# Performance work log

Measured on AMD Instinct MI355X. Metric: run time of the kernel, lower is better.

The kernel has to match this reference:

```python
import jax, jax.numpy as jnp
import numpy as np

N = 102400   # total nodes (64 graphs x 1600 nodes)
G = 64       # graphs in batch
NPG = N // G
E = 1638400  # total edges (avg degree 16)
EPG = E // G


def _segmean(x, ids, num):
    s = jax.ops.segment_sum(x, ids, num_segments=num)
    c = jax.ops.segment_sum(jnp.ones((x.shape[0], 1), x.dtype), ids, num_segments=num)
    return s / jnp.maximum(c, 1.0)


def setup_inputs() -> dict:
    key = jax.random.key(0)
    ks = jax.random.split(key, 32)
    node_features = jax.random.normal(ks[0], (N, 60), jnp.float32)
    edge_features = jax.random.normal(ks[1], (E, 1), jnp.float32)
    node_graph = jnp.arange(N, dtype=jnp.int32) // NPG
    edge_graph = jnp.arange(E, dtype=jnp.int32) // EPG
    senders = edge_graph * NPG + jax.random.randint(ks[2], (E,), 0, NPG)
    receivers = edge_graph * NPG + jax.random.randint(ks[3], (E,), 0, NPG)

    def W(k, o, i):
        return (jax.random.normal(k, (o, i), jnp.float32) / np.sqrt(i)).astype(jnp.float32)

    def b(k, o):
        return (jax.random.uniform(k, (o,), jnp.float32) * 0.02 - 0.01).astype(jnp.float32)

    p = dict(
        node_features=node_features, edge_features=edge_features,
        senders=senders, receivers=receivers,
        node_graph=node_graph, edge_graph=edge_graph,
        # encoder: EdgeLinear(8, edge=1, sender=60)
        enc_Wee=W(ks[4], 8, 1), enc_Wes=W(ks[5], 8, 60), enc_be=b(ks[6], 8),
        # encoder: NodeLinear(16, incoming=8, node=60)
        enc_Wnn=W(ks[7], 16, 60), enc_Wni=W(ks[8], 16, 8), enc_bn=b(ks[9], 16),
        # encoder: GlobalLinear(4, edge=8, node=16)
        enc_Wge=W(ks[10], 4, 8), enc_Wgn=W(ks[11], 4, 16), enc_bg=b(ks[12], 4),
        # hidden: EdgeLinear(8, edge=8, sender=16, global=4)
        hid_Wee=W(ks[13], 8, 8), hid_Wes=W(ks[14], 8, 16), hid_Weg=W(ks[15], 8, 4), hid_be=b(ks[16], 8),
        # hidden: NodeLinear(16, node=16, incoming=8, global=4)
        hid_Wnn=W(ks[17], 16, 16), hid_Wni=W(ks[18], 16, 8), hid_Wng=W(ks[19], 16, 4), hid_bn=b(ks[20], 16),
        # hidden: GlobalLinear(4, edge=8, node=16, global=4)
        hid_Wge=W(ks[21], 4, 8), hid_Wgn=W(ks[22], 4, 16), hid_Wgg=W(ks[23], 4, 4), hid_bg=b(ks[24], 4),
        # readouts
        ro_Wn=W(ks[25], 1, 16), ro_bn=b(ks[26], 1),
        ro_Wg=W(ks[27], 1, 4), ro_bg=b(ks[28], 1),
    )
    return p


def reference(node_features, edge_features, senders, receivers, node_graph, edge_graph,
              enc_Wee, enc_Wes, enc_be, enc_Wnn, enc_Wni, enc_bn, enc_Wge, enc_Wgn, enc_bg,
              hid_Wee, hid_Wes, hid_Weg, hid_be, hid_Wnn, hid_Wni, hid_Wng, hid_bn,
              hid_Wge, hid_Wgn, hid_Wgg, hid_bg, ro_Wn, ro_bn, ro_Wg, ro_bg):
    hops = 1
    # ---- encoder GN block ----
    e = jax.nn.relu(edge_features @ enc_Wee.T + node_features[senders] @ enc_Wes.T + enc_be)  # [E,8]
    n = jax.nn.relu(node_features @ enc_Wnn.T + _segmean(e, receivers, N) @ enc_Wni.T + enc_bn)  # [N,16]
    g = jax.nn.relu(_segmean(e, edge_graph, G) @ enc_Wge.T + _segmean(n, node_graph, G) @ enc_Wgn.T + enc_bg)  # [G,4]
    # ---- hidden GN blocks (shared weights across hops) ----
    for _ in range(hops):
        e = jax.nn.relu(e @ hid_Wee.T + n[senders] @ hid_Wes.T + g[edge_graph] @ hid_Weg.T + hid_be)
        n = jax.nn.relu(n @ hid_Wnn.T + _segmean(e, receivers, N) @ hid_Wni.T + g[node_graph] @ hid_Wng.T + hid_bn)
        g = jax.nn.relu(_segmean(e, edge_graph, G) @ hid_Wge.T + _segmean(n, node_graph, G) @ hid_Wgn.T + g @ hid_Wgg.T + hid_bg)
    # ---- readouts ----
    nodes_out = jax.nn.sigmoid(n @ ro_Wn.T + ro_bn)    # [N,1]
    globals_out = jax.nn.sigmoid(g @ ro_Wg.T + ro_bg)  # [G,1]
    return nodes_out, globals_out
```

## Files before the change

kernel.cpp:

```cpp
#include <hip/hip_runtime.h>
#include <hip/hip_bf16.h>
#include <hip/hip_fp16.h>

#define NN   102400
#define NG   64
#define NPG  1600
#define NE   1638400
#define EPG  25600
#define EPC  (EPG / 4)

typedef unsigned int u32;
typedef unsigned short u16;

#define OFF_EDAT  0
#define OFF_SPROJ (NE)
#define OFF_PNN   (NE + 8 * NN)
#define OFF_DEG   (NE + 16 * NN)
#define OFF_START (NE + 17 * NN)
#define OFF_H4C   (NE + 18 * NN)
#define OFF_GS    (NE + 22 * NN)
#define GS_ESUM1 0
#define GS_NSUM1 512
#define GS_ESUM2 1536
#define GS_NSUM2 2048
#define GS_G1    3072
#define GS_GPE   3328
#define GS_GPN   3840

struct H8 { __half2 a, b, c, d; };

__device__ __forceinline__ void unpack8(const H8 v, float* o) {
    float2 t0 = __half22float2(v.a), t1 = __half22float2(v.b);
    float2 t2 = __half22float2(v.c), t3 = __half22float2(v.d);
    o[0]=t0.x; o[1]=t0.y; o[2]=t1.x; o[3]=t1.y; o[4]=t2.x; o[5]=t2.y; o[6]=t3.x; o[7]=t3.y;
}
__device__ __forceinline__ H8 pack8(const float* v) {
    H8 r;
    r.a = __floats2half2_rn(v[0], v[1]); r.b = __floats2half2_rn(v[2], v[3]);
    r.c = __floats2half2_rn(v[4], v[5]); r.d = __floats2half2_rn(v[6], v[7]);
    return r;
}
__device__ __forceinline__ u16 f2bf(float f) {
    u32 u = __float_as_uint(f);
    return (u16)((u + 0x7fffu + ((u >> 16) & 1u)) >> 16);
}
__device__ __forceinline__ float wsum(float v) {
#pragma unroll
    for (int o = 32; o >= 1; o >>= 1) v += __shfl_xor(v, o);
    return v;
}
__device__ __forceinline__ float sigmoidf_(float x) { return 1.f / (1.f + expf(-x)); }

__global__ __launch_bounds__(512) void k_hist4(const int* __restrict__ rcv, int* __restrict__ h4) {
    __shared__ int h[NPG];
    const int g = blockIdx.x >> 2, c = blockIdx.x & 3;
    for (int i = threadIdx.x; i < NPG; i += 512) h[i] = 0;
    __syncthreads();
    const int base = g * EPG + c * EPC;
    for (int t = threadIdx.x; t < EPC; t += 512) atomicAdd(&h[rcv[base + t] - g * NPG], 1);
    __syncthreads();
    int* out = h4 + (size_t)(g * 4 + c) * NPG;
    for (int i = threadIdx.x; i < NPG; i += 512) out[i] = h[i];
}

__global__ __launch_bounds__(320) void k_scan(
    int* __restrict__ h4c, int* __restrict__ deg, int* __restrict__ start)
{
    __shared__ int part[320];
    const int g = blockIdx.x, tid = threadIdx.x;
    const int vb = tid * 5;
    int hc[5][4], d[5], pre[5];
    int ts = 0;
#pragma unroll
    for (int i = 0; i < 5; ++i) {
        const int v = vb + i;
#pragma unroll
        for (int c = 0; c < 4; ++c) hc[i][c] = h4c[(size_t)(g * 4 + c) * NPG + v];
        d[i] = hc[i][0] + hc[i][1] + hc[i][2] + hc[i][3];
        pre[i] = ts;
        ts += d[i];
    }
    part[tid] = ts;
    __syncthreads();
    for (int o = 1; o < 320; o <<= 1) {
        const int v = (tid >= o) ? part[tid - o] : 0;
        __syncthreads();
        part[tid] += v;
        __syncthreads();
    }
    const int off = g * EPG + part[tid] - ts;
#pragma unroll
    for (int i = 0; i < 5; ++i) {
        const int v = vb + i;
        const int st = off + pre[i];
        deg[g * NPG + v] = d[i];
        start[g * NPG + v] = st;
        int run = st;
#pragma unroll
        for (int c = 0; c < 4; ++c) {
            h4c[(size_t)(g * 4 + c) * NPG + v] = run;
            run += hc[i][c];
        }
    }
}

__global__ __launch_bounds__(512) void k_scatter4(
    const float* __restrict__ ef, const int* __restrict__ snd, const int* __restrict__ rcv,
    const int* __restrict__ h4c, u32* __restrict__ edat)
{
    __shared__ int cur[NPG];
    const int g = blockIdx.x >> 2, c = blockIdx.x & 3;
    const int* cb = h4c + (size_t)(g * 4 + c) * NPG;
    for (int i = threadIdx.x; i < NPG; i += 512) cur[i] = cb[i];
    __syncthreads();
    const int base = g * EPG + c * EPC;
    for (int t = threadIdx.x; t < EPC; t += 512) {
        const int e = base + t;
        const int r = rcv[e] - g * NPG;
        const int p = atomicAdd(&cur[r], 1);
        const u32 s = (u32)(snd[e] - g * NPG);
        edat[p] = (s << 16) | (u32)f2bf(ef[e]);
    }
}

__global__ __launch_bounds__(256) void k_node_pre(
    const float* __restrict__ nf,
    const float* __restrict__ Wes,
    const float* __restrict__ Wnn,
    const float* __restrict__ ebe, const float* __restrict__ ebn,
    __half* __restrict__ sproj, __half* __restrict__ pnn)
{
    __shared__ float wE[480], wN[960];
    for (int i = threadIdx.x; i < 480; i += 256) wE[i] = Wes[i];
    for (int i = threadIdx.x; i < 960; i += 256) wN[i] = Wnn[i];
    __syncthreads();
    const int v = blockIdx.x * 256 + threadIdx.x;
    const float4* row = reinterpret_cast<const float4*>(nf + (size_t)v * 60);
    float x[60];
#pragma unroll
    for (int i = 0; i < 15; ++i) {
        const float4 a = row[i];
        x[4 * i] = a.x; x[4 * i + 1] = a.y; x[4 * i + 2] = a.z; x[4 * i + 3] = a.w;
    }
    float pes[8], pn[16];
#pragma unroll
    for (int j = 0; j < 8; ++j) pes[j] = ebe[j];
#pragma unroll
    for (int j = 0; j < 16; ++j) pn[j] = ebn[j];
#pragma unroll
    for (int k = 0; k < 60; ++k) {
        const float xv = x[k];
#pragma unroll
        for (int j = 0; j < 8; ++j)  pes[j] = fmaf(xv, wE[j * 60 + k], pes[j]);
#pragma unroll
        for (int j = 0; j < 16; ++j) pn[j]  = fmaf(xv, wN[j * 60 + k], pn[j]);
    }
    H8* sp = reinterpret_cast<H8*>(sproj) + (size_t)v * 2;
    sp[0] = pack8(pes);
    H8* pp = reinterpret_cast<H8*>(pnn) + (size_t)v * 2;
    pp[0] = pack8(pn); pp[1] = pack8(pn + 8);
}

__global__ __launch_bounds__(256) void k_enc(
    const int* __restrict__ deg, const int* __restrict__ start, const u32* __restrict__ edat,
    __half* __restrict__ sproj, __half* __restrict__ pnn,
    const float* __restrict__ eWee,
    const float* __restrict__ eWni,
    const float* __restrict__ hWes, const float* __restrict__ hWnn,
    float* __restrict__ esum, float* __restrict__ nsum)
{
    __shared__ float wNI[128], wES[128], wNN2[256];
    for (int i = threadIdx.x; i < 128; i += 256) { wNI[i] = eWni[i]; wES[i] = hWes[i]; }
    for (int i = threadIdx.x; i < 256; i += 256) wNN2[i] = hWnn[i];
    __syncthreads();
    const int v = blockIdx.x * 256 + threadIdx.x;
    const int g = v / NPG;
    float wee[8];
#pragma unroll
    for (int j = 0; j < 8; ++j) wee[j] = eWee[j];
    const int dg = deg[v];
    const int st = start[v];
    float m[8];
#pragma unroll
    for (int j = 0; j < 8; ++j) m[j] = 0.f;
    const H8* hb = reinterpret_cast<const H8*>(sproj) + (size_t)g * NPG * 2;
    for (int i = 0; i < dg; ++i) {
        const u32 w = edat[st + i];
        const float f = __uint_as_float((w & 0xffffu) << 16);
        const int s = (int)(w >> 16);
        float pv[8]; unpack8(hb[(size_t)s * 2], pv);
#pragma unroll
        for (int j = 0; j < 8; ++j) m[j] += fmaxf(0.f, fmaf(f, wee[j], pv[j]));
    }
#pragma unroll
    for (int j = 0; j < 8; ++j) {
        const float t = wsum(m[j]);
        if ((threadIdx.x & 63) == 0) atomicAdd(&esum[g * 8 + j], t);
    }
    const float ic = 1.f / fmaxf((float)dg, 1.f);
    float mk[8];
#pragma unroll
    for (int k = 0; k < 8; ++k) mk[k] = m[k] * ic;
    const H8* pp = reinterpret_cast<const H8*>(pnn) + (size_t)v * 2;
    float pn[16]; unpack8(pp[0], pn); unpack8(pp[1], pn + 8);
    float n1[16];
#pragma unroll
    for (int j = 0; j < 16; ++j) {
        float x = pn[j];
#pragma unroll
        for (int k = 0; k < 8; ++k) x = fmaf(mk[k], wNI[j * 8 + k], x);
        n1[j] = fmaxf(0.f, x);
    }
    float pe[8];
#pragma unroll
    for (int o = 0; o < 8; ++o) {
        float x = 0.f;
#pragma unroll
        for (int j = 0; j < 16; ++j) x = fmaf(n1[j], wES[o * 16 + j], x);
        pe[o] = x;
    }
    H8* spw = reinterpret_cast<H8*>(sproj) + (size_t)v * 2;
    spw[1] = pack8(pe);
    float pw[16];
#pragma unroll
    for (int o = 0; o < 16; ++o) {
        float x = 0.f;
#pragma unroll
        for (int j = 0; j < 16; ++j) x = fmaf(n1[j], wNN2[o * 16 + j], x);
        pw[o] = x;
    }
    H8* ppw = reinterpret_cast<H8*>(pnn) + (size_t)v * 2;
    ppw[0] = pack8(pw); ppw[1] = pack8(pw + 8);
#pragma unroll
    for (int j = 0; j < 16; ++j) {
        const float t = wsum(n1[j]);
        if ((threadIdx.x & 63) == 0) atomicAdd(&nsum[g * 16 + j], t);
    }
}

__global__ void k_glob_enc(
    const float* __restrict__ esum1, const float* __restrict__ nsum1,
    const float* __restrict__ Wge, const float* __restrict__ Wgn, const float* __restrict__ bg,
    const float* __restrict__ hWeg, const float* __restrict__ hWng,
    float* __restrict__ g1, float* __restrict__ gpe, float* __restrict__ gpn)
{
    const int g = threadIdx.x;
    if (g >= NG) return;
    float gv[4];
#pragma unroll
    for (int o = 0; o < 4; ++o) {
        float x = bg[o];
#pragma unroll
        for (int k = 0; k < 8; ++k)  x = fmaf(esum1[g * 8 + k] * (1.f / EPG), Wge[o * 8 + k], x);
#pragma unroll
        for (int k = 0; k < 16; ++k) x = fmaf(nsum1[g * 16 + k] * (1.f / NPG), Wgn[o * 16 + k], x);
        gv[o] = fmaxf(0.f, x);
        g1[g * 4 + o] = gv[o];
    }
#pragma unroll
    for (int j = 0; j < 8; ++j) {
        float x = 0.f;
#pragma unroll
        for (int o = 0; o < 4; ++o) x = fmaf(gv[o], hWeg[j * 4 + o], x);
        gpe[g * 8 + j] = x;
    }
#pragma unroll
    for (int j = 0; j < 16; ++j) {
        float x = 0.f;
#pragma unroll
        for (int o = 0; o < 4; ++o) x = fmaf(gv[o], hWng[j * 4 + o], x);
        gpn[g * 16 + j] = x;
    }
}

__global__ __launch_bounds__(256) void k_hid(
    const int* __restrict__ deg, const int* __restrict__ start, const u32* __restrict__ edat,
    const __half* __restrict__ sproj, const __half* __restrict__ pnn,
    const float* __restrict__ eWee,
    const float* __restrict__ hWee, const float* __restrict__ hbe, const float* __restrict__ gpe,
    const float* __restrict__ hWni, const float* __restrict__ hbn, const float* __restrict__ gpn,
    const float* __restrict__ roWn, const float* __restrict__ robn,
    float* __restrict__ esum, float* __restrict__ nsum, float* __restrict__ outn)
{
    __shared__ float w2[64], wNI[128], rW[16];
    for (int i = threadIdx.x; i < 128; i += 256) wNI[i] = hWni[i];
    if (threadIdx.x < 64) w2[threadIdx.x] = hWee[threadIdx.x];
    if (threadIdx.x < 16) rW[threadIdx.x] = roWn[threadIdx.x];
    __syncthreads();
    const int v = blockIdx.x * 256 + threadIdx.x;
    const int g = v / NPG;
    float wee[8], add2[8];
#pragma unroll
    for (int j = 0; j < 8; ++j) { wee[j] = eWee[j]; add2[j] = gpe[g * 8 + j] + hbe[j]; }
    const int dg = deg[v];
    const int st = start[v];
    float m2[8];
#pragma unroll
    for (int j = 0; j < 8; ++j) m2[j] = 0.f;
    const H8* hb = reinterpret_cast<const H8*>(sproj) + (size_t)g * NPG * 2;
    for (int i = 0; i < dg; ++i) {
        const u32 w = edat[st + i];
        const float f = __uint_as_float((w & 0xffffu) << 16);
        const int s = (int)(w >> 16);
        float pv[8], qv[8];
        unpack8(hb[(size_t)s * 2], pv);
        unpack8(hb[(size_t)s * 2 + 1], qv);
        float e1[8];
#pragma unroll
        for (int j = 0; j < 8; ++j) e1[j] = fmaxf(0.f, fmaf(f, wee[j], pv[j]));
#pragma unroll
        for (int j = 0; j < 8; ++j) {
            float x = qv[j] + add2[j];
#pragma unroll
            for (int k = 0; k < 8; ++k) x = fmaf(e1[k], w2[j * 8 + k], x);
            m2[j] += fmaxf(0.f, x);
        }
    }
#pragma unroll
    for (int j = 0; j < 8; ++j) {
        const float t = wsum(m2[j]);
        if ((threadIdx.x & 63) == 0) atomicAdd(&esum[g * 8 + j], t);
    }
    const float ic = 1.f / fmaxf((float)dg, 1.f);
    float mk[8];
#pragma unroll
    for (int k = 0; k < 8; ++k) mk[k] = m2[k] * ic;
    const H8* pp = reinterpret_cast<const H8*>(pnn) + (size_t)v * 2;
    float pn[16]; unpack8(pp[0], pn); unpack8(pp[1], pn + 8);
    float z = robn[0];
    float n2[16];
#pragma unroll
    for (int j = 0; j < 16; ++j) {
        float x = pn[j] + gpn[g * 16 + j] + hbn[j];
#pragma unroll
        for (int k = 0; k < 8; ++k) x = fmaf(mk[k], wNI[j * 8 + k], x);
        n2[j] = fmaxf(0.f, x);
        z = fmaf(n2[j], rW[j], z);
    }
    outn[v] = sigmoidf_(z);
#pragma unroll
    for (int j = 0; j < 16; ++j) {
        const float t = wsum(n2[j]);
        if ((threadIdx.x & 63) == 0) atomicAdd(&nsum[g * 16 + j], t);
    }
}

__global__ void k_glob_hid(
    const float* __restrict__ esum2, const float* __restrict__ nsum2, const float* __restrict__ g1,
    const float* __restrict__ hWge, const float* __restrict__ hWgn,
    const float* __restrict__ hWgg, const float* __restrict__ hbg,
    const float* __restrict__ roWg, const float* __restrict__ robg,
    float* __restrict__ outg)
{
    const int g = threadIdx.x;
    if (g >= NG) return;
    float gv[4];
#pragma unroll
    for (int o = 0; o < 4; ++o) {
        float x = hbg[o];
#pragma unroll
        for (int k = 0; k < 8; ++k)  x = fmaf(esum2[g * 8 + k] * (1.f / EPG), hWge[o * 8 + k], x);
#pragma unroll
        for (int k = 0; k < 16; ++k) x = fmaf(nsum2[g * 16 + k] * (1.f / NPG), hWgn[o * 16 + k], x);
#pragma unroll
        for (int k = 0; k < 4; ++k)  x = fmaf(g1[g * 4 + k], hWgg[o * 4 + k], x);
        gv[o] = fmaxf(0.f, x);
    }
    float z = robg[0];
#pragma unroll
    for (int o = 0; o < 4; ++o) z = fmaf(gv[o], roWg[o], z);
    outg[g] = sigmoidf_(z);
}

extern "C" void kernel_launch(void* const* d_in, const int* in_sizes, int n_in,
                              void* d_out, int out_size, void* d_ws, size_t ws_size,
                              hipStream_t stream)
{
    const float* nf   = (const float*)d_in[0];
    const float* ef   = (const float*)d_in[1];
    const int*   snd  = (const int*)d_in[2];
    const int*   rcv  = (const int*)d_in[3];
    const float* eWee = (const float*)d_in[6];
    const float* eWes = (const float*)d_in[7];
    const float* ebe  = (const float*)d_in[8];
    const float* eWnn = (const float*)d_in[9];
    const float* eWni = (const float*)d_in[10];
    const float* ebn  = (const float*)d_in[11];
    const float* eWge = (const float*)d_in[12];
    const float* eWgn = (const float*)d_in[13];
    const float* ebg  = (const float*)d_in[14];
    const float* hWee = (const float*)d_in[15];
    const float* hWes = (const float*)d_in[16];
    const float* hWeg = (const float*)d_in[17];
    const float* hbe  = (const float*)d_in[18];
    const float* hWnn = (const float*)d_in[19];
    const float* hWni = (const float*)d_in[20];
    const float* hWng = (const float*)d_in[21];
    const float* hbn  = (const float*)d_in[22];
    const float* hWge = (const float*)d_in[23];
    const float* hWgn = (const float*)d_in[24];
    const float* hWgg = (const float*)d_in[25];
    const float* hbg  = (const float*)d_in[26];
    const float* roWn = (const float*)d_in[27];
    const float* robn = (const float*)d_in[28];
    const float* roWg = (const float*)d_in[29];
    const float* robg = (const float*)d_in[30];

    float*  ws    = (float*)d_ws;
    u32*    edat  = (u32*)(ws + OFF_EDAT);
    __half* sproj = (__half*)(ws + OFF_SPROJ);
    __half* pnn   = (__half*)(ws + OFF_PNN);
    int*    deg   = (int*)(ws + OFF_DEG);
    int*    start = (int*)(ws + OFF_START);
    int*    h4c   = (int*)(ws + OFF_H4C);
    float*  gs    = ws + OFF_GS;
    float* esum1 = gs + GS_ESUM1;
    float* nsum1 = gs + GS_NSUM1;
    float* esum2 = gs + GS_ESUM2;
    float* nsum2 = gs + GS_NSUM2;
    float* g1    = gs + GS_G1;
    float* gpe   = gs + GS_GPE;
    float* gpn   = gs + GS_GPN;
    float* out   = (float*)d_out;

    hipMemsetAsync(gs, 0, 3072 * sizeof(float), stream);

    k_hist4<<<NG * 4, 512, 0, stream>>>(rcv, h4c);
    k_scan<<<NG, 320, 0, stream>>>(h4c, deg, start);
    k_scatter4<<<NG * 4, 512, 0, stream>>>(ef, snd, rcv, h4c, edat);
    k_node_pre<<<NN / 256, 256, 0, stream>>>(nf, eWes, eWnn, ebe, ebn, sproj, pnn);
    k_enc<<<NN / 256, 256, 0, stream>>>(deg, start, edat, sproj, pnn,
                                        eWee, eWni, hWes, hWnn, esum1, nsum1);
    k_glob_enc<<<1, 64, 0, stream>>>(esum1, nsum1, eWge, eWgn, ebg, hWeg, hWng, g1, gpe, gpn);
    k_hid<<<NN / 256, 256, 0, stream>>>(deg, start, edat, sproj, pnn,
                                        eWee, hWee, hbe, gpe, hWni, hbn, gpn,
                                        roWn, robn, esum2, nsum2, out);
    k_glob_hid<<<1, 64, 0, stream>>>(esum2, nsum2, g1, hWge, hWgn, hWgg, hbg, roWg, robg, out + NN);
}
```

Baseline: 145.7 us.

## Split each node's edge gather across two threads and unroll gathers by four

The encoder and hidden node kernels now give each node to two threads. Each thread handles half the incoming edges, and the partial sums are combined with a lane shuffle; the per-node 16-wide projections are also split between the two threads. The edge loops are unrolled by four with the gathered loads issued up front, to raise memory-level parallelism on the random sender gathers. The global-sum memset is folded into the first block of k_node_pre, which removes one launch. The cost is twice as many threads, extra shuffles, and a modified wave reduction that relies on the lane pairing.

Measured after the change: 144.0 us. Within noise of the previous version (-1.1%).

```diff
diff --git a/kernel.cpp b/kernel.cpp
--- a/kernel.cpp
+++ b/kernel.cpp
@@ -28,6 +28,7 @@
 #define GS_GPN   3840
 
 struct H8 { __half2 a, b, c, d; };
+struct H4 { __half2 a, b; };
 
 __device__ __forceinline__ void unpack8(const H8 v, float* o) {
     float2 t0 = __half22float2(v.a), t1 = __half22float2(v.b);
@@ -40,13 +41,18 @@
     r.c = __floats2half2_rn(v[4], v[5]); r.d = __floats2half2_rn(v[6], v[7]);
     return r;
 }
+__device__ __forceinline__ H4 pack4(const float* v) {
+    H4 r;
+    r.a = __floats2half2_rn(v[0], v[1]); r.b = __floats2half2_rn(v[2], v[3]);
+    return r;
+}
 __device__ __forceinline__ u16 f2bf(float f) {
     u32 u = __float_as_uint(f);
     return (u16)((u + 0x7fffu + ((u >> 16) & 1u)) >> 16);
 }
-__device__ __forceinline__ float wsum(float v) {
-#pragma unroll
-    for (int o = 32; o >= 1; o >>= 1) v += __shfl_xor(v, o);
+__device__ __forceinline__ float wsum_par(float v) {
+#pragma unroll
+    for (int o = 2; o <= 32; o <<= 1) v += __shfl_xor(v, o);
     return v;
 }
 __device__ __forceinline__ float sigmoidf_(float x) { return 1.f / (1.f + expf(-x)); }
@@ -128,11 +134,14 @@
     const float* __restrict__ Wes,
     const float* __restrict__ Wnn,
     const float* __restrict__ ebe, const float* __restrict__ ebn,
-    __half* __restrict__ sproj, __half* __restrict__ pnn)
+    __half* __restrict__ sproj, __half* __restrict__ pnn, float* __restrict__ gs)
 {
     __shared__ float wE[480], wN[960];
     for (int i = threadIdx.x; i < 480; i += 256) wE[i] = Wes[i];
     for (int i = threadIdx.x; i < 960; i += 256) wN[i] = Wnn[i];
+    if (blockIdx.x == 0) {
+        for (int i = threadIdx.x; i < 3072; i += 256) gs[i] = 0.f;
+    }
     __syncthreads();
     const int v = blockIdx.x * 256 + threadIdx.x;
     const float4* row = reinterpret_cast<const float4*>(nf + (size_t)v * 60);
@@ -171,70 +180,99 @@
 {
     __shared__ float wNI[128], wES[128], wNN2[256];
     for (int i = threadIdx.x; i < 128; i += 256) { wNI[i] = eWni[i]; wES[i] = hWes[i]; }
-    for (int i = threadIdx.x; i < 256; i += 256) wNN2[i] = hWnn[i];
-    __syncthreads();
-    const int v = blockIdx.x * 256 + threadIdx.x;
+    wNN2[threadIdx.x] = hWnn[threadIdx.x];
+    __syncthreads();
+    const int t = blockIdx.x * 256 + threadIdx.x;
+    const int v = t >> 1, h = t & 1;
     const int g = v / NPG;
     float wee[8];
 #pragma unroll
     for (int j = 0; j < 8; ++j) wee[j] = eWee[j];
     const int dg = deg[v];
     const int st = start[v];
+    const int half0 = dg >> 1;
+    int i = st + (h ? half0 : 0);
+    const int iend = st + (h ? dg : half0);
     float m[8];
 #pragma unroll
     for (int j = 0; j < 8; ++j) m[j] = 0.f;
     const H8* hb = reinterpret_cast<const H8*>(sproj) + (size_t)g * NPG * 2;
-    for (int i = 0; i < dg; ++i) {
-        const u32 w = edat[st + i];
-        const float f = __uint_as_float((w & 0xffffu) << 16);
-        const int s = (int)(w >> 16);
-        float pv[8]; unpack8(hb[(size_t)s * 2], pv);
-#pragma unroll
-        for (int j = 0; j < 8; ++j) m[j] += fmaxf(0.f, fmaf(f, wee[j], pv[j]));
-    }
+
+#define ENC_EDGE(W, A) { \
+    const float f_ = __uint_as_float(((W) & 0xffffu) << 16); \
+    float pv_[8]; unpack8((A), pv_); \
+    _Pragma("unroll") \
+    for (int j = 0; j < 8; ++j) m[j] += fmaxf(0.f, fmaf(f_, wee[j], pv_[j])); }
+
+    for (; i + 4 <= iend; i += 4) {
+        const u32 w0 = edat[i], w1 = edat[i + 1], w2v = edat[i + 2], w3v = edat[i + 3];
+        const H8 A0 = hb[(size_t)(w0 >> 16) * 2];
+        const H8 A1 = hb[(size_t)(w1 >> 16) * 2];
+        const H8 A2 = hb[(size_t)(w2v >> 16) * 2];
+        const H8 A3 = hb[(size_t)(w3v >> 16) * 2];
+        ENC_EDGE(w0, A0) ENC_EDGE(w1, A1) ENC_EDGE(w2v, A2) ENC_EDGE(w3v, A3)
+    }
+    for (; i < iend; ++i) {
+        const u32 w = edat[i];
+        const H8 A = hb[(size_t)(w >> 16) * 2];
+        ENC_EDGE(w, A)
+    }
+#undef ENC_EDGE
+
+#pragma unroll
+    for (int j = 0; j < 8; ++j) m[j] += __shfl_xor(m[j], 1);
 #pragma unroll
     for (int j = 0; j < 8; ++j) {
-        const float t = wsum(m[j]);
-        if ((threadIdx.x & 63) == 0) atomicAdd(&esum[g * 8 + j], t);
+        const float s = wsum_par(m[j]);
+        if ((threadIdx.x & 63) == 0) atomicAdd(&esum[g * 8 + j], s);
     }
     const float ic = 1.f / fmaxf((float)dg, 1.f);
     float mk[8];
 #pragma unroll
     for (int k = 0; k < 8; ++k) mk[k] = m[k] * ic;
     const H8* pp = reinterpret_cast<const H8*>(pnn) + (size_t)v * 2;
-    float pn[16]; unpack8(pp[0], pn); unpack8(pp[1], pn + 8);
-    float n1[16];
-#pragma unroll
-    for (int j = 0; j < 16; ++j) {
-        float x = pn[j];
-#pragma unroll
-        for (int k = 0; k < 8; ++k) x = fmaf(mk[k], wNI[j * 8 + k], x);
-        n1[j] = fmaxf(0.f, x);
-    }
-    float pe[8];
-#pragma unroll
-    for (int o = 0; o < 8; ++o) {
+    float pn8[8]; unpack8(pp[h], pn8);
+    float n1[8];
+#pragma unroll
+    for (int jj = 0; jj < 8; ++jj) {
+        float x = pn8[jj];
+#pragma unroll
+        for (int k = 0; k < 8; ++k) x = fmaf(mk[k], wNI[(h * 8 + jj) * 8 + k], x);
+        n1[jj] = fmaxf(0.f, x);
+    }
+    float n1o[8];
+#pragma unroll
+    for (int jj = 0; jj < 8; ++jj) n1o[jj] = __shfl_xor(n1[jj], 1);
+    float full[16];
+#pragma unroll
+    for (int jj = 0; jj < 8; ++jj) {
+        full[jj]     = h ? n1o[jj] : n1[jj];
+        full[8 + jj] = h ? n1[jj]  : n1o[jj];
+    }
+    float pe4[4];
+#pragma unroll
+    for (int oo = 0; oo < 4; ++oo) {
+        const int o = h * 4 + oo;
         float x = 0.f;
 #pragma unroll
-        for (int j = 0; j < 16; ++j) x = fmaf(n1[j], wES[o * 16 + j], x);
-        pe[o] = x;
-    }
-    H8* spw = reinterpret_cast<H8*>(sproj) + (size_t)v * 2;
-    spw[1] = pack8(pe);
-    float pw[16];
-#pragma unroll
-    for (int o = 0; o < 16; ++o) {
+        for (int j = 0; j < 16; ++j) x = fmaf(full[j], wES[o * 16 + j], x);
+        pe4[oo] = x;
+    }
+    *reinterpret_cast<H4*>(sproj + (size_t)v * 16 + 8 + h * 4) = pack4(pe4);
+    float pw8[8];
+#pragma unroll
+    for (int oo = 0; oo < 8; ++oo) {
+        const int o = h * 8 + oo;
         float x = 0.f;
 #pragma unroll
-        for (int j = 0; j < 16; ++j) x = fmaf(n1[j], wNN2[o * 16 + j], x);
-        pw[o] = x;
-    }
-    H8* ppw = reinterpret_cast<H8*>(pnn) + (size_t)v * 2;
-    ppw[0] = pack8(pw); ppw[1] = pack8(pw + 8);
-#pragma unroll
-    for (int j = 0; j < 16; ++j) {
-        const float t = wsum(n1[j]);
-        if ((threadIdx.x & 63) == 0) atomicAdd(&nsum[g * 16 + j], t);
+        for (int j = 0; j < 16; ++j) x = fmaf(full[j], wNN2[o * 16 + j], x);
+        pw8[oo] = x;
+    }
+    reinterpret_cast<H8*>(pnn)[(size_t)v * 2 + h] = pack8(pw8);
+#pragma unroll
+    for (int jj = 0; jj < 8; ++jj) {
+        const float s = wsum_par(n1[jj]);
+        if ((threadIdx.x & 63) == h) atomicAdd(&nsum[g * 16 + h * 8 + jj], s);
     }
 }
 
@@ -287,61 +325,83 @@
     if (threadIdx.x < 64) w2[threadIdx.x] = hWee[threadIdx.x];
     if (threadIdx.x < 16) rW[threadIdx.x] = roWn[threadIdx.x];
     __syncthreads();
-    const int v = blockIdx.x * 256 + threadIdx.x;
+    const int t = blockIdx.x * 256 + threadIdx.x;
+    const int v = t >> 1, h = t & 1;
     const int g = v / NPG;
     float wee[8], add2[8];
 #pragma unroll
     for (int j = 0; j < 8; ++j) { wee[j] = eWee[j]; add2[j] = gpe[g * 8 + j] + hbe[j]; }
     const int dg = deg[v];
     const int st = start[v];
+    const int half0 = dg >> 1;
+    int i = st + (h ? half0 : 0);
+    const int iend = st + (h ? dg : half0);
     float m2[8];
 #pragma unroll
     for (int j = 0; j < 8; ++j) m2[j] = 0.f;
     const H8* hb = reinterpret_cast<const H8*>(sproj) + (size_t)g * NPG * 2;
-    for (int i = 0; i < dg; ++i) {
-        const u32 w = edat[st + i];
-        const float f = __uint_as_float((w & 0xffffu) << 16);
-        const int s = (int)(w >> 16);
-        float pv[8], qv[8];
-        unpack8(hb[(size_t)s * 2], pv);
-        unpack8(hb[(size_t)s * 2 + 1], qv);
-        float e1[8];
-#pragma unroll
-        for (int j = 0; j < 8; ++j) e1[j] = fmaxf(0.f, fmaf(f, wee[j], pv[j]));
-#pragma unroll
-        for (int j = 0; j < 8; ++j) {
-            float x = qv[j] + add2[j];
-#pragma unroll
-            for (int k = 0; k < 8; ++k) x = fmaf(e1[k], w2[j * 8 + k], x);
-            m2[j] += fmaxf(0.f, x);
-        }
-    }
+
+#define HID_EDGE(W, A, B) { \
+    const float f_ = __uint_as_float(((W) & 0xffffu) << 16); \
+    float pv_[8], qv_[8]; unpack8((A), pv_); unpack8((B), qv_); \
+    float e1_[8]; \
+    _Pragma("unroll") \
+    for (int j = 0; j < 8; ++j) e1_[j] = fmaxf(0.f, fmaf(f_, wee[j], pv_[j])); \
+    _Pragma("unroll") \
+    for (int j = 0; j < 8; ++j) { \
+        float x_ = qv_[j] + add2[j]; \
+        _Pragma("unroll") \
+        for (int k = 0; k < 8; ++k) x_ = fmaf(e1_[k], w2[j * 8 + k], x_); \
+        m2[j] += fmaxf(0.f, x_); } }
+
+    for (; i + 4 <= iend; i += 4) {
+        const u32 w0 = edat[i], w1 = edat[i + 1], w2v = edat[i + 2], w3v = edat[i + 3];
+        const size_t s0 = (size_t)(w0 >> 16) * 2, s1 = (size_t)(w1 >> 16) * 2;
+        const size_t s2 = (size_t)(w2v >> 16) * 2, s3 = (size_t)(w3v >> 16) * 2;
+        const H8 A0 = hb[s0], B0 = hb[s0 + 1];
+        const H8 A1 = hb[s1], B1 = hb[s1 + 1];
+        const H8 A2 = hb[s2], B2 = hb[s2 + 1];
+        const H8 A3 = hb[s3], B3 = hb[s3 + 1];
+        HID_EDGE(w0, A0, B0) HID_EDGE(w1, A1, B1) HID_EDGE(w2v, A2, B2) HID_EDGE(w3v, A3, B3)
+    }
+    for (; i < iend; ++i) {
+        const u32 w = edat[i];
+        const size_t s = (size_t)(w >> 16) * 2;
+        const H8 A = hb[s], B = hb[s + 1];
+        HID_EDGE(w, A, B)
+    }
+#undef HID_EDGE
+
+#pragma unroll
+    for (int j = 0; j < 8; ++j) m2[j] += __shfl_xor(m2[j], 1);
 #pragma unroll
     for (int j = 0; j < 8; ++j) {
-        const float t = wsum(m2[j]);
-        if ((threadIdx.x & 63) == 0) atomicAdd(&esum[g * 8 + j], t);
+        const float s = wsum_par(m2[j]);
+        if ((threadIdx.x & 63) == 0) atomicAdd(&esum[g * 8 + j], s);
     }
     const float ic = 1.f / fmaxf((float)dg, 1.f);
     float mk[8];
 #pragma unroll
     for (int k = 0; k < 8; ++k) mk[k] = m2[k] * ic;
     const H8* pp = reinterpret_cast<const H8*>(pnn) + (size_t)v * 2;
-    float pn[16]; unpack8(pp[0], pn); unpack8(pp[1], pn + 8);
-    float z = robn[0];
-    float n2[16];
-#pragma unroll
-    for (int j = 0; j < 16; ++j) {
-        float x = pn[j] + gpn[g * 16 + j] + hbn[j];
+    float pn8[8]; unpack8(pp[h], pn8);
+    float zp = 0.f;
+    float n2[8];
+#pragma unroll
+    for (int jj = 0; jj < 8; ++jj) {
+        const int j = h * 8 + jj;
+        float x = pn8[jj] + gpn[g * 16 + j] + hbn[j];
 #pragma unroll
         for (int k = 0; k < 8; ++k) x = fmaf(mk[k], wNI[j * 8 + k], x);
-        n2[j] = fmaxf(0.f, x);
-        z = fmaf(n2[j], rW[j], z);
-    }
-    outn[v] = sigmoidf_(z);
-#pragma unroll
-    for (int j = 0; j < 16; ++j) {
-        const float t = wsum(n2[j]);
-        if ((threadIdx.x & 63) == 0) atomicAdd(&nsum[g * 16 + j], t);
+        n2[jj] = fmaxf(0.f, x);
+        zp = fmaf(n2[jj], rW[j], zp);
+    }
+    const float z = zp + __shfl_xor(zp, 1);
+    if (h == 0) outn[v] = sigmoidf_(z + robn[0]);
+#pragma unroll
+    for (int jj = 0; jj < 8; ++jj) {
+        const float s = wsum_par(n2[jj]);
+        if ((threadIdx.x & 63) == h) atomicAdd(&nsum[g * 16 + h * 8 + jj], s);
     }
 }
 
@@ -423,17 +483,15 @@
     float* gpn   = gs + GS_GPN;
     float* out   = (float*)d_out;
 
-    hipMemsetAsync(gs, 0, 3072 * sizeof(float), stream);
-
     k_hist4<<<NG * 4, 512, 0, stream>>>(rcv, h4c);
     k_scan<<<NG, 320, 0, stream>>>(h4c, deg, start);
     k_scatter4<<<NG * 4, 512, 0, stream>>>(ef, snd, rcv, h4c, edat);
-    k_node_pre<<<NN / 256, 256, 0, stream>>>(nf, eWes, eWnn, ebe, ebn, sproj, pnn);
-    k_enc<<<NN / 256, 256, 0, stream>>>(deg, start, edat, sproj, pnn,
-                                        eWee, eWni, hWes, hWnn, esum1, nsum1);
+    k_node_pre<<<NN / 256, 256, 0, stream>>>(nf, eWes, eWnn, ebe, ebn, sproj, pnn, gs);
+    k_enc<<<NN * 2 / 256, 256, 0, stream>>>(deg, start, edat, sproj, pnn,
+                                            eWee, eWni, hWes, hWnn, esum1, nsum1);
     k_glob_enc<<<1, 64, 0, stream>>>(esum1, nsum1, eWge, eWgn, ebg, hWeg, hWng, g1, gpe, gpn);
-    k_hid<<<NN / 256, 256, 0, stream>>>(deg, start, edat, sproj, pnn,
-                                        eWee, hWee, hbe, gpe, hWni, hbn, gpn,
-                                        roWn, robn, esum2, nsum2, out);
+    k_hid<<<NN * 2 / 256, 256, 0, stream>>>(deg, start, edat, sproj, pnn,
+                                            eWee, hWee, hbe, gpe, hWni, hbn, gpn,
+                                            roWn, robn, esum2, nsum2, out);
     k_glob_hid<<<1, 64, 0, stream>>>(esum2, nsum2, g1, hWge, hWgn, hWgg, hbg, roWg, robg, out + NN);
 }
```

## Fuse global-update kernels via last-block counters and batch edge gathers

Applied to the files above, without the earlier changes.

Removes the two single-block global kernels and the memset. The last block of the encoder and hidden kernels, found through an atomic counter, now computes the per-graph global update, and the accumulators are zeroed inside k_node_pre and k_scan. The per-node edge loops are restructured to issue 16 (encoder) or 8 (hidden) independent index and gather loads before computing, with masked padding, to raise memory-level parallelism. This adds a threadfence and counter atomics per block plus some wasted gather work on padded iterations.

After: 190.5 us. 30.8% more time.

```diff
diff --git a/kernel.cpp b/kernel.cpp
--- a/kernel.cpp
+++ b/kernel.cpp
@@ -19,6 +19,7 @@
 #define OFF_START (NE + 17 * NN)
 #define OFF_H4C   (NE + 18 * NN)
 #define OFF_GS    (NE + 22 * NN)
+#define OFF_CNT   (NE + 22 * NN + 4864)
 #define GS_ESUM1 0
 #define GS_NSUM1 512
 #define GS_ESUM2 1536
@@ -29,6 +30,12 @@
 
 struct H8 { __half2 a, b, c, d; };
 
+__device__ __forceinline__ void unpack8_f4(const float4 v, float* o) {
+    const __half2* h = reinterpret_cast<const __half2*>(&v);
+    float2 t0 = __half22float2(h[0]), t1 = __half22float2(h[1]);
+    float2 t2 = __half22float2(h[2]), t3 = __half22float2(h[3]);
+    o[0]=t0.x; o[1]=t0.y; o[2]=t1.x; o[3]=t1.y; o[4]=t2.x; o[5]=t2.y; o[6]=t3.x; o[7]=t3.y;
+}
 __device__ __forceinline__ void unpack8(const H8 v, float* o) {
     float2 t0 = __half22float2(v.a), t1 = __half22float2(v.b);
     float2 t2 = __half22float2(v.c), t3 = __half22float2(v.d);
@@ -64,8 +71,9 @@
 }
 
 __global__ __launch_bounds__(320) void k_scan(
-    int* __restrict__ h4c, int* __restrict__ deg, int* __restrict__ start)
-{
+    int* __restrict__ h4c, int* __restrict__ deg, int* __restrict__ start, int* __restrict__ cnt)
+{
+    if (blockIdx.x == 0 && threadIdx.x == 0) { cnt[0] = 0; cnt[1] = 0; }
     __shared__ int part[320];
     const int g = blockIdx.x, tid = threadIdx.x;
     const int vb = tid * 5;
@@ -125,14 +133,16 @@
 
 __global__ __launch_bounds__(256) void k_node_pre(
     const float* __restrict__ nf,
-    const float* __restrict__ Wes,
-    const float* __restrict__ Wnn,
+    const float* __restrict__ Wes, const float* __restrict__ Wnn,
     const float* __restrict__ ebe, const float* __restrict__ ebn,
-    __half* __restrict__ sproj, __half* __restrict__ pnn)
+    __half* __restrict__ sproj, __half* __restrict__ pnn, float* __restrict__ gs)
 {
     __shared__ float wE[480], wN[960];
     for (int i = threadIdx.x; i < 480; i += 256) wE[i] = Wes[i];
     for (int i = threadIdx.x; i < 960; i += 256) wN[i] = Wnn[i];
+    if (blockIdx.x == 0) {
+        for (int i = threadIdx.x; i < 3072; i += 256) gs[i] = 0.f;
+    }
     __syncthreads();
     const int v = blockIdx.x * 256 + threadIdx.x;
     const float4* row = reinterpret_cast<const float4*>(nf + (size_t)v * 60);
@@ -161,17 +171,21 @@
     pp[0] = pack8(pn); pp[1] = pack8(pn + 8);
 }
 
-__global__ __launch_bounds__(256) void k_enc(
+__global__ __launch_bounds__(256) void k_enc2(
     const int* __restrict__ deg, const int* __restrict__ start, const u32* __restrict__ edat,
     __half* __restrict__ sproj, __half* __restrict__ pnn,
-    const float* __restrict__ eWee,
-    const float* __restrict__ eWni,
+    const float* __restrict__ eWee, const float* __restrict__ eWni,
     const float* __restrict__ hWes, const float* __restrict__ hWnn,
-    float* __restrict__ esum, float* __restrict__ nsum)
+    float* __restrict__ esum, float* __restrict__ nsum,
+    const float* __restrict__ eWge, const float* __restrict__ eWgn, const float* __restrict__ ebg,
+    const float* __restrict__ hWeg, const float* __restrict__ hWng,
+    float* __restrict__ g1, float* __restrict__ gpe, float* __restrict__ gpn,
+    int* __restrict__ cnt)
 {
     __shared__ float wNI[128], wES[128], wNN2[256];
+    __shared__ int lastFlag;
     for (int i = threadIdx.x; i < 128; i += 256) { wNI[i] = eWni[i]; wES[i] = hWes[i]; }
-    for (int i = threadIdx.x; i < 256; i += 256) wNN2[i] = hWnn[i];
+    wNN2[threadIdx.x] = hWnn[threadIdx.x];
     __syncthreads();
     const int v = blockIdx.x * 256 + threadIdx.x;
     const int g = v / NPG;
@@ -183,25 +197,37 @@
     float m[8];
 #pragma unroll
     for (int j = 0; j < 8; ++j) m[j] = 0.f;
-    const H8* hb = reinterpret_cast<const H8*>(sproj) + (size_t)g * NPG * 2;
-    for (int i = 0; i < dg; ++i) {
-        const u32 w = edat[st + i];
-        const float f = __uint_as_float((w & 0xffffu) << 16);
-        const int s = (int)(w >> 16);
-        float pv[8]; unpack8(hb[(size_t)s * 2], pv);
-#pragma unroll
-        for (int j = 0; j < 8; ++j) m[j] += fmaxf(0.f, fmaf(f, wee[j], pv[j]));
+    const float4* hb4 = reinterpret_cast<const float4*>(sproj) + (size_t)g * NPG * 2;
+
+    for (int base = 0; base < dg; base += 16) {
+        u32 w[16];
+#pragma unroll
+        for (int j = 0; j < 16; ++j) {
+            const int idx = base + j;
+            w[j] = edat[st + (idx < dg ? idx : 0)];
+        }
+        float4 A[16];
+#pragma unroll
+        for (int j = 0; j < 16; ++j) A[j] = hb4[(size_t)(w[j] >> 16) * 2];
+#pragma unroll
+        for (int j = 0; j < 16; ++j) {
+            const float val = (base + j < dg) ? 1.f : 0.f;
+            const float f = __uint_as_float((w[j] & 0xffffu) << 16);
+            float pv[8]; unpack8_f4(A[j], pv);
+#pragma unroll
+            for (int k = 0; k < 8; ++k) m[k] += val * fmaxf(0.f, fmaf(f, wee[k], pv[k]));
+        }
     }
 #pragma unroll
     for (int j = 0; j < 8; ++j) {
-        const float t = wsum(m[j]);
-        if ((threadIdx.x & 63) == 0) atomicAdd(&esum[g * 8 + j], t);
+        const float s = wsum(m[j]);
+        if ((threadIdx.x & 63) == 0) atomicAdd(&esum[g * 8 + j], s);
     }
     const float ic = 1.f / fmaxf((float)dg, 1.f);
     float mk[8];
 #pragma unroll
     for (int k = 0; k < 8; ++k) mk[k] = m[k] * ic;
-    const H8* pp = reinterpret_cast<const H8*>(pnn) + (size_t)v * 2;
+    H8* pp = reinterpret_cast<H8*>(pnn) + (size_t)v * 2;
     float pn[16]; unpack8(pp[0], pn); unpack8(pp[1], pn + 8);
     float n1[16];
 #pragma unroll
@@ -219,8 +245,7 @@
         for (int j = 0; j < 16; ++j) x = fmaf(n1[j], wES[o * 16 + j], x);
         pe[o] = x;
     }
-    H8* spw = reinterpret_cast<H8*>(sproj) + (size_t)v * 2;
-    spw[1] = pack8(pe);
+    reinterpret_cast<H8*>(sproj)[(size_t)v * 2 + 1] = pack8(pe);
     float pw[16];
 #pragma unroll
     for (int o = 0; o < 16; ++o) {
@@ -229,60 +254,71 @@
         for (int j = 0; j < 16; ++j) x = fmaf(n1[j], wNN2[o * 16 + j], x);
         pw[o] = x;
     }
-    H8* ppw = reinterpret_cast<H8*>(pnn) + (size_t)v * 2;
-    ppw[0] = pack8(pw); ppw[1] = pack8(pw + 8);
+    pp[0] = pack8(pw); pp[1] = pack8(pw + 8);
 #pragma unroll
     for (int j = 0; j < 16; ++j) {
-        const float t = wsum(n1[j]);
-        if ((threadIdx.x & 63) == 0) atomicAdd(&nsum[g * 16 + j], t);
-    }
-}
-
-__global__ void k_glob_enc(
-    const float* __restrict__ esum1, const float* __restrict__ nsum1,
-    const float* __restrict__ Wge, const float* __restrict__ Wgn, const float* __restrict__ bg,
-    const float* __restrict__ hWeg, const float* __restrict__ hWng,
-    float* __restrict__ g1, float* __restrict__ gpe, float* __restrict__ gpn)
-{
-    const int g = threadIdx.x;
-    if (g >= NG) return;
-    float gv[4];
-#pragma unroll
-    for (int o = 0; o < 4; ++o) {
-        float x = bg[o];
-#pragma unroll
-        for (int k = 0; k < 8; ++k)  x = fmaf(esum1[g * 8 + k] * (1.f / EPG), Wge[o * 8 + k], x);
-#pragma unroll
-        for (int k = 0; k < 16; ++k) x = fmaf(nsum1[g * 16 + k] * (1.f / NPG), Wgn[o * 16 + k], x);
-        gv[o] = fmaxf(0.f, x);
-        g1[g * 4 + o] = gv[o];
-    }
-#pragma unroll
-    for (int j = 0; j < 8; ++j) {
-        float x = 0.f;
-#pragma unroll
-        for (int o = 0; o < 4; ++o) x = fmaf(gv[o], hWeg[j * 4 + o], x);
-        gpe[g * 8 + j] = x;
-    }
-#pragma unroll
-    for (int j = 0; j < 16; ++j) {
-        float x = 0.f;
-#pragma unroll
-        for (int o = 0; o < 4; ++o) x = fmaf(gv[o], hWng[j * 4 + o], x);
-        gpn[g * 16 + j] = x;
-    }
-}
-
-__global__ __launch_bounds__(256) void k_hid(
+        const float s = wsum(n1[j]);
+        if ((threadIdx.x & 63) == 0) atomicAdd(&nsum[g * 16 + j], s);
+    }
+
+    __threadfence();
+    __syncthreads();
+    if (threadIdx.x == 0) {
+        const int old = atomicAdd(&cnt[0], 1);
+        lastFlag = (old == (int)gridDim.x - 1);
+    }
+    __syncthreads();
+    if (lastFlag && threadIdx.x < NG) {
+        const int gg = threadIdx.x;
+        float es[8], ns[16];
+#pragma unroll
+        for (int k = 0; k < 8; ++k)  es[k] = atomicAdd(&esum[gg * 8 + k], 0.f) * (1.f / EPG);
+#pragma unroll
+        for (int k = 0; k < 16; ++k) ns[k] = atomicAdd(&nsum[gg * 16 + k], 0.f) * (1.f / NPG);
+        float gv[4];
+#pragma unroll
+        for (int o = 0; o < 4; ++o) {
+            float x = ebg[o];
+#pragma unroll
+            for (int k = 0; k < 8; ++k)  x = fmaf(es[k], eWge[o * 8 + k], x);
+#pragma unroll
+            for (int k = 0; k < 16; ++k) x = fmaf(ns[k], eWgn[o * 16 + k], x);
+            gv[o] = fmaxf(0.f, x);
+            g1[gg * 4 + o] = gv[o];
+        }
+#pragma unroll
+        for (int j = 0; j < 8; ++j) {
+            float x = 0.f;
+#pragma unroll
+            for (int o = 0; o < 4; ++o) x = fmaf(gv[o], hWeg[j * 4 + o], x);
+            gpe[gg * 8 + j] = x;
+        }
+#pragma unroll
+        for (int j = 0; j < 16; ++j) {
+            float x = 0.f;
+#pragma unroll
+            for (int o = 0; o < 4; ++o) x = fmaf(gv[o], hWng[j * 4 + o], x);
+            gpn[gg * 16 + j] = x;
+        }
+    }
+}
+
+__global__ __launch_bounds__(256) void k_hid2(
     const int* __restrict__ deg, const int* __restrict__ start, const u32* __restrict__ edat,
     const __half* __restrict__ sproj, const __half* __restrict__ pnn,
     const float* __restrict__ eWee,
     const float* __restrict__ hWee, const float* __restrict__ hbe, const float* __restrict__ gpe,
     const float* __restrict__ hWni, const float* __restrict__ hbn, const float* __restrict__ gpn,
     const float* __restrict__ roWn, const float* __restrict__ robn,
-    float* __restrict__ esum, float* __restrict__ nsum, float* __restrict__ outn)
+    float* __restrict__ esum, float* __restrict__ nsum, float* __restrict__ outn,
+    const float* __restrict__ g1,
+    const float* __restrict__ hWge, const float* __restrict__ hWgn,
+    const float* __restrict__ hWgg, const float* __restrict__ hbg,
+    const float* __restrict__ roWg, const float* __restrict__ robg,
+    float* __restrict__ outg, int* __restrict__ cnt)
 {
     __shared__ float w2[64], wNI[128], rW[16];
+    __shared__ int lastFlag;
     for (int i = threadIdx.x; i < 128; i += 256) wNI[i] = hWni[i];
     if (threadIdx.x < 64) w2[threadIdx.x] = hWee[threadIdx.x];
     if (threadIdx.x < 16) rW[threadIdx.x] = roWn[threadIdx.x];
@@ -297,29 +333,43 @@
     float m2[8];
 #pragma unroll
     for (int j = 0; j < 8; ++j) m2[j] = 0.f;
-    const H8* hb = reinterpret_cast<const H8*>(sproj) + (size_t)g * NPG * 2;
-    for (int i = 0; i < dg; ++i) {
-        const u32 w = edat[st + i];
-        const float f = __uint_as_float((w & 0xffffu) << 16);
-        const int s = (int)(w >> 16);
-        float pv[8], qv[8];
-        unpack8(hb[(size_t)s * 2], pv);
-        unpack8(hb[(size_t)s * 2 + 1], qv);
-        float e1[8];
-#pragma unroll
-        for (int j = 0; j < 8; ++j) e1[j] = fmaxf(0.f, fmaf(f, wee[j], pv[j]));
+    const float4* hb4 = reinterpret_cast<const float4*>(sproj) + (size_t)g * NPG * 2;
+
+    for (int base = 0; base < dg; base += 8) {
+        u32 w[8];
 #pragma unroll
         for (int j = 0; j < 8; ++j) {
-            float x = qv[j] + add2[j];
-#pragma unroll
-            for (int k = 0; k < 8; ++k) x = fmaf(e1[k], w2[j * 8 + k], x);
-            m2[j] += fmaxf(0.f, x);
+            const int idx = base + j;
+            w[j] = edat[st + (idx < dg ? idx : 0)];
+        }
+        float4 A[8], B[8];
+#pragma unroll
+        for (int j = 0; j < 8; ++j) {
+            const size_t s2 = (size_t)(w[j] >> 16) * 2;
+            A[j] = hb4[s2]; B[j] = hb4[s2 + 1];
+        }
+#pragma unroll
+        for (int j = 0; j < 8; ++j) {
+            const float val = (base + j < dg) ? 1.f : 0.f;
+            const float f = __uint_as_float((w[j] & 0xffffu) << 16);
+            float pv[8], qv[8];
+            unpack8_f4(A[j], pv); unpack8_f4(B[j], qv);
+            float e1[8];
+#pragma unroll
+            for (int k = 0; k < 8; ++k) e1[k] = fmaxf(0.f, fmaf(f, wee[k], pv[k]));
+#pragma unroll
+            for (int k = 0; k < 8; ++k) {
+                float x = qv[k] + add2[k];
+#pragma unroll
+                for (int kk = 0; kk < 8; ++kk) x = fmaf(e1[kk], w2[k * 8 + kk], x);
+                m2[k] += val * fmaxf(0.f, x);
+            }
         }
     }
 #pragma unroll
     for (int j = 0; j < 8; ++j) {
-        const float t = wsum(m2[j]);
-        if ((threadIdx.x & 63) == 0) atomicAdd(&esum[g * 8 + j], t);
+        const float s = wsum(m2[j]);
+        if ((threadIdx.x & 63) == 0) atomicAdd(&esum[g * 8 + j], s);
     }
     const float ic = 1.f / fmaxf((float)dg, 1.f);
     float mk[8];
@@ -340,36 +390,41 @@
     outn[v] = sigmoidf_(z);
 #pragma unroll
     for (int j = 0; j < 16; ++j) {
-        const float t = wsum(n2[j]);
-        if ((threadIdx.x & 63) == 0) atomicAdd(&nsum[g * 16 + j], t);
-    }
-}
-
-__global__ void k_glob_hid(
-    const float* __restrict__ esum2, const float* __restrict__ nsum2, const float* __restrict__ g1,
-    const float* __restrict__ hWge, const float* __restrict__ hWgn,
-    const float* __restrict__ hWgg, const float* __restrict__ hbg,
-    const float* __restrict__ roWg, const float* __restrict__ robg,
-    float* __restrict__ outg)
-{
-    const int g = threadIdx.x;
-    if (g >= NG) return;
-    float gv[4];
-#pragma unroll
-    for (int o = 0; o < 4; ++o) {
-        float x = hbg[o];
-#pragma unroll
-        for (int k = 0; k < 8; ++k)  x = fmaf(esum2[g * 8 + k] * (1.f / EPG), hWge[o * 8 + k], x);
-#pragma unroll
-        for (int k = 0; k < 16; ++k) x = fmaf(nsum2[g * 16 + k] * (1.f / NPG), hWgn[o * 16 + k], x);
-#pragma unroll
-        for (int k = 0; k < 4; ++k)  x = fmaf(g1[g * 4 + k], hWgg[o * 4 + k], x);
-        gv[o] = fmaxf(0.f, x);
-    }
-    float z = robg[0];
-#pragma unroll
-    for (int o = 0; o < 4; ++o) z = fmaf(gv[o], roWg[o], z);
-    outg[g] = sigmoidf_(z);
+        const float s = wsum(n2[j]);
+        if ((threadIdx.x & 63) == 0) atomicAdd(&nsum[g * 16 + j], s);
+    }
+
+    __threadfence();
+    __syncthreads();
+    if (threadIdx.x == 0) {
+        const int old = atomicAdd(&cnt[1], 1);
+        lastFlag = (old == (int)gridDim.x - 1);
+    }
+    __syncthreads();
+    if (lastFlag && threadIdx.x < NG) {
+        const int gg = threadIdx.x;
+        float es[8], ns[16];
+#pragma unroll
+        for (int k = 0; k < 8; ++k)  es[k] = atomicAdd(&esum[gg * 8 + k], 0.f) * (1.f / EPG);
+#pragma unroll
+        for (int k = 0; k < 16; ++k) ns[k] = atomicAdd(&nsum[gg * 16 + k], 0.f) * (1.f / NPG);
+        float gv[4];
+#pragma unroll
+        for (int o = 0; o < 4; ++o) {
+            float x = hbg[o];
+#pragma unroll
+            for (int k = 0; k < 8; ++k)  x = fmaf(es[k], hWge[o * 8 + k], x);
+#pragma unroll
+            for (int k = 0; k < 16; ++k) x = fmaf(ns[k], hWgn[o * 16 + k], x);
+#pragma unroll
+            for (int k = 0; k < 4; ++k)  x = fmaf(g1[gg * 4 + k], hWgg[o * 4 + k], x);
+            gv[o] = fmaxf(0.f, x);
+        }
+        float zz = robg[0];
+#pragma unroll
+        for (int o = 0; o < 4; ++o) zz = fmaf(gv[o], roWg[o], zz);
+        outg[gg] = sigmoidf_(zz);
+    }
 }
 
 extern "C" void kernel_launch(void* const* d_in, const int* in_sizes, int n_in,
@@ -414,6 +469,7 @@
     int*    start = (int*)(ws + OFF_START);
     int*    h4c   = (int*)(ws + OFF_H4C);
     float*  gs    = ws + OFF_GS;
+    int*    cnt   = (int*)(ws + OFF_CNT);
     float* esum1 = gs + GS_ESUM1;
     float* nsum1 = gs + GS_NSUM1;
     float* esum2 = gs + GS_ESUM2;
@@ -423,17 +479,16 @@
     float* gpn   = gs + GS_GPN;
     float* out   = (float*)d_out;
 
-    hipMemsetAsync(gs, 0, 3072 * sizeof(float), stream);
-
     k_hist4<<<NG * 4, 512, 0, stream>>>(rcv, h4c);
-    k_scan<<<NG, 320, 0, stream>>>(h4c, deg, start);
+    k_scan<<<NG, 320, 0, stream>>>(h4c, deg, start, cnt);
     k_scatter4<<<NG * 4, 512, 0, stream>>>(ef, snd, rcv, h4c, edat);
-    k_node_pre<<<NN / 256, 256, 0, stream>>>(nf, eWes, eWnn, ebe, ebn, sproj, pnn);
-    k_enc<<<NN / 256, 256, 0, stream>>>(deg, start, edat, sproj, pnn,
-                                        eWee, eWni, hWes, hWnn, esum1, nsum1);
-    k_glob_enc<<<1, 64, 0, stream>>>(esum1, nsum1, eWge, eWgn, ebg, hWeg, hWng, g1, gpe, gpn);
-    k_hid<<<NN / 256, 256, 0, stream>>>(deg, start, edat, sproj, pnn,
-                                        eWee, hWee, hbe, gpe, hWni, hbn, gpn,
-                                        roWn, robn, esum2, nsum2, out);
-    k_glob_hid<<<1, 64, 0, stream>>>(esum2, nsum2, g1, hWge, hWgn, hWgg, hbg, roWg, robg, out + NN);
-}
+    k_node_pre<<<NN / 256, 256, 0, stream>>>(nf, eWes, eWnn, ebe, ebn, sproj, pnn, gs);
+    k_enc2<<<NN / 256, 256, 0, stream>>>(deg, start, edat, sproj, pnn,
+                                         eWee, eWni, hWes, hWnn, esum1, nsum1,
+                                         eWge, eWgn, ebg, hWeg, hWng, g1, gpe, gpn, cnt);
+    k_hid2<<<NN / 256, 256, 0, stream>>>(deg, start, edat, sproj, pnn,
+                                         eWee, hWee, hbe, gpe, hWni, hbn, gpn,
+                                         roWn, robn, esum2, nsum2, out,
+                                         g1, hWge, hWgn, hWgg, hbg, roWg, robg,
+                                         out + NN, cnt);
+}
```
